# Kernel tuning notes

Hardware: AMD Instinct MI355X
Metric: run time of the kernel (lower is better)

The kernel has to match this reference:

```python
import jax, jax.numpy as jnp
from jax import lax
import numpy as np

N, H, K, B, L = 8192, 256, 100, 32, 128
FS = [1, 2, 3, 4]
W2 = 2 * H + 10  # conv kernel width; padded input width (2H+10) == kernel width -> out width 1


def setup_inputs() -> dict:
    key = jax.random.key(0)
    ks = jax.random.split(key, 16)
    inp = {}
    # scale adj by 1/sqrt(N) so layer1 activations stay O(1) (keeps softmax numerically sane)
    inp["adj"] = jax.random.normal(ks[0], (N, N), jnp.float32) / np.float32(np.sqrt(N))
    # xavier-uniform-scale init for the node embedding parameter
    inp["embedding"] = jax.random.normal(ks[1], (N, H), jnp.float32) * np.float32(np.sqrt(2.0 / (N + H)))
    inp["q_idx"] = jax.random.randint(ks[2], (B, L), 0, N, dtype=jnp.int32)
    inp["a_idx"] = jax.random.randint(ks[3], (B, L), 0, N, dtype=jnp.int32)
    for i, fs in enumerate(FS):
        fan_in = fs * W2
        inp[f"conv_w{i}"] = jax.random.normal(ks[4 + i], (K, 1, fs, W2), jnp.float32) / np.float32(np.sqrt(fan_in))
        inp[f"conv_b{i}"] = jnp.zeros((K,), jnp.float32)
    inp["dense_w"] = jax.random.normal(ks[12], (4 * K * 2, 2), jnp.float32) * np.float32(0.02)
    inp["dense_b"] = jnp.zeros((2,), jnp.float32)
    return inp


def _cnn_branch(t, conv_ws, conv_bs):
    # t: [B, 1, L, 2H]; each conv has padding=5 on both spatial dims,
    # kernel width == 2H+10 so output width == 1; relu then max-pool over full height.
    outs = []
    for w, b in zip(conv_ws, conv_bs):
        y = lax.conv_general_dilated(t, w, (1, 1), [(5, 5), (5, 5)],
                                     dimension_numbers=("NCHW", "OIHW", "NCHW"))
        y = jax.nn.relu(y + b[None, :, None, None])  # [B, K, L+10-fs+1, 1]
        outs.append(jnp.max(y, axis=(2, 3)))  # [B, K]
    return jnp.concatenate(outs, axis=1)  # [B, 4K]


def reference(adj, embedding, q_idx, a_idx,
              conv_w0, conv_b0, conv_w1, conv_b1,
              conv_w2, conv_b2, conv_w3, conv_b3,
              dense_w, dense_b):
    conv_ws = [conv_w0, conv_w1, conv_w2, conv_w3]
    conv_bs = [conv_b0, conv_b1, conv_b2, conv_b3]
    # featureless GCN layer: layer1 = A @ E  -> [N, H]
    layer1 = adj @ embedding
    # per-sample word gathers (ragged in original, fixed length L here)
    Q = layer1[q_idx]  # [B, L, H]
    A = layer1[a_idx]  # [B, L, H]
    # soft alignment: score = Q A^T; wq = softmax rows; wa = softmax(score.T, dim=1) == softmax over axis 1
    score = jnp.einsum("blh,bmh->blm", Q, A)
    wq = jax.nn.softmax(score, axis=2)
    wa = jax.nn.softmax(score, axis=1)
    EQ = jnp.einsum("blm,bmh->blh", wq, A)  # aligned encoding of Q
    EA = jnp.einsum("blm,blh->bmh", wa, Q)  # aligned encoding of A
    # match features: squared diff ++ elementwise product -> [B, 1, L, 2H]
    tq = jnp.concatenate([(Q - EQ) ** 2, Q * EQ], axis=-1)[:, None]
    ta = jnp.concatenate([(A - EA) ** 2, A * EA], axis=-1)[:, None]
    # dropout is identity in eval mode
    q_re = jax.nn.relu(_cnn_branch(tq, conv_ws, conv_bs))  # [B, 4K]
    a_re = jax.nn.relu(_cnn_branch(ta, conv_ws, conv_bs))  # [B, 4K]
    re = jnp.concatenate([q_re, a_re], axis=1)  # [B, 8K]
    logits = re @ dense_w + dense_b  # [B, 2]  (F.relu(score) in original is a discarded no-op)
    return jax.nn.log_softmax(logits, axis=1)
```

## Files before the change

### kernel.cpp

```cpp
#include <hip/hip_runtime.h>
#include <hip/hip_bf16.h>
#include <stdint.h>

typedef unsigned short u16;
typedef __attribute__((ext_vector_type(8))) short bf16x8;
typedef __attribute__((ext_vector_type(4))) float f32x4;

#define NN 8192
#define HH 256
#define KK 100
#define BB 32
#define LL 128
#define SPLITK 8
#define KCH (NN / SPLITK)
#define STEPS1 (KCH / 64)
#define WCATR 1120

__device__ __forceinline__ u16 f2bf_rne(float x) {
  union { __hip_bfloat16 h; u16 u; } v;
  v.h = __float2bfloat16(x);
  return v.u;
}

__device__ __forceinline__ float bf2f(u16 u) {
  union { unsigned int i; float f; } v;
  v.i = ((unsigned int)u) << 16;
  return v.f;
}

__device__ __forceinline__ bf16x8 pack8(f32x4 a, f32x4 b) {
  bf16x8 r;
  r[0] = (short)f2bf_rne(a.x); r[1] = (short)f2bf_rne(a.y);
  r[2] = (short)f2bf_rne(a.z); r[3] = (short)f2bf_rne(a.w);
  r[4] = (short)f2bf_rne(b.x); r[5] = (short)f2bf_rne(b.y);
  r[6] = (short)f2bf_rne(b.z); r[7] = (short)f2bf_rne(b.w);
  return r;
}

__device__ __forceinline__ void gld16(const void* g, void* l) {
  __builtin_amdgcn_global_load_lds(
      (const __attribute__((address_space(1))) unsigned int*)g,
      (__attribute__((address_space(3))) unsigned int*)l, 16, 0, 0);
}

__global__ __launch_bounds__(256) void prep_all(const float* __restrict__ emb,
                                                u16* __restrict__ embT,
                                                const float* __restrict__ w0,
                                                const float* __restrict__ w1,
                                                const float* __restrict__ w2,
                                                const float* __restrict__ w3,
                                                u16* __restrict__ Wcat,
                                                const int* __restrict__ q_idx,
                                                const int* __restrict__ a_idx,
                                                int* __restrict__ rank,
                                                int* __restrict__ rows,
                                                int* __restrict__ muniq) {
  const int bid = blockIdx.x;
  const int tid = threadIdx.x;
  if (bid < 512) {
    __shared__ float t[64][65];
    const int k0 = (bid & 127) * 64, n0 = (bid >> 7) * 64;
#pragma unroll
    for (int i = 0; i < 16; ++i) {
      int idx = i * 256 + tid;
      int r = idx >> 6, c = idx & 63;
      t[r][c] = emb[(size_t)(k0 + r) * HH + n0 + c];
    }
    __syncthreads();
#pragma unroll
    for (int i = 0; i < 16; ++i) {
      int idx = i * 256 + tid;
      int r = idx >> 6, c = idx & 63;
      embT[(size_t)(n0 + r) * NN + k0 + c] = f2bf_rne(t[c][r]);
    }
  } else if (bid < 512 + WCATR) {
    const int kr = bid - 512;
    u16* out = Wcat + (size_t)kr * 512;
    if (kr >= KK * 10) {
      out[tid] = 0;
      out[tid + 256] = 0;
      return;
    }
    const int k = kr / 10, s = kr % 10;
    const float* w;
    int r, fs;
    if (s < 1)      { w = w0; r = s;     fs = 1; }
    else if (s < 3) { w = w1; r = s - 1; fs = 2; }
    else if (s < 6) { w = w2; r = s - 3; fs = 3; }
    else            { w = w3; r = s - 6; fs = 4; }
    const float* src = w + ((size_t)k * fs + r) * 522 + 5;
    out[tid] = f2bf_rne(src[tid]);
    out[tid + 256] = f2bf_rne(src[tid + 256]);
  } else {
    __shared__ unsigned bm[256];
    __shared__ int cnt[256];
    bm[tid] = 0u;
    __syncthreads();
    for (int i = tid; i < BB * LL; i += 256) {
      int q = q_idx[i];
      atomicOr(&bm[q >> 5], 1u << (q & 31));
    }
    for (int i = tid; i < BB * LL; i += 256) {
      int a = a_idx[i];
      atomicOr(&bm[a >> 5], 1u << (a & 31));
    }
    __syncthreads();
    const unsigned w = bm[tid];
    const int myc = __popc(w);
    cnt[tid] = myc;
    __syncthreads();
    for (int off = 1; off < 256; off <<= 1) {
      int v = (tid >= off) ? cnt[tid - off] : 0;
      __syncthreads();
      cnt[tid] += v;
      __syncthreads();
    }
    const int total = cnt[255];
    int base = cnt[tid] - myc;
    for (int j = 0; j < 32; ++j) {
      int n = tid * 32 + j;
      rank[n] = base;
      if ((w >> j) & 1) rows[base++] = n;
    }
    __syncthreads();
    if (tid == 0) *muniq = total;
    if (tid < 128) rows[total + tid] = 0;
  }
}

__global__ __launch_bounds__(512, 6) void gemm_layer1c(const float* __restrict__ adj,
                                                       const u16* __restrict__ embT,
                                                       const int* __restrict__ rows,
                                                       const int* __restrict__ muniq,
                                                       u16* __restrict__ parts) {
  __shared__ __align__(16) float As[64 * 64];
  __shared__ __align__(16) u16 Bs[256 * 64];
  const int tid = threadIdx.x;
  const int lane = tid & 63, wid = tid >> 6;
  const int wm = wid >> 2, wn = wid & 3;
  const int wg = blockIdx.x;
  const int sk = wg & 7;
  const int mt = wg >> 3;
  const int m0 = mt * 64;
  const int M = *muniq;
  if (m0 >= M) return;
  const int kbeg = sk * KCH;

  f32x4 acc[2][4];
  const f32x4 zf = {0.f, 0.f, 0.f, 0.f};
#pragma unroll
  for (int i = 0; i < 2; ++i)
#pragma unroll
    for (int j = 0; j < 4; ++j) acc[i][j] = zf;

  int aRowLoc[2], aGsrc[2];
  const float* aSrc[2];
#pragma unroll
  for (int j = 0; j < 2; ++j) {
    int t = wid * 2 + j;
    aRowLoc[j] = t * 4 + (lane >> 4);
    aGsrc[j] = (lane & 15) ^ (aRowLoc[j] & 15);
    int grow = rows[m0 + aRowLoc[j]];
    aSrc[j] = adj + (size_t)grow * NN + kbeg + aGsrc[j] * 4;
  }
  const u16* bSrc[4];
#pragma unroll
  for (int j = 0; j < 4; ++j) {
    int t = wid * 4 + j;
    int rowB = t * 8 + (lane >> 3);
    int g = (lane & 7) ^ (rowB & 7);
    bSrc[j] = embT + (size_t)rowB * NN + kbeg + g * 8;
  }

  for (int s = 0; s < STEPS1; ++s) {
    const int ks = s * 64;
#pragma unroll
    for (int j = 0; j < 2; ++j)
      gld16(aSrc[j] + ks, (void*)&As[(wid * 2 + j) * 256]);
#pragma unroll
    for (int j = 0; j < 4; ++j)
      gld16(bSrc[j] + ks, (void*)&Bs[(wid * 4 + j) * 512]);
    __syncthreads();
#pragma unroll
    for (int kk = 0; kk < 64; kk += 32) {
      bf16x8 af[2], bfr[4];
      const int g0 = (kk >> 2) + ((lane >> 4) << 1);
#pragma unroll
      for (int mi = 0; mi < 2; ++mi) {
        int row = wm * 32 + mi * 16 + (lane & 15);
        f32x4 p0 = *reinterpret_cast<const f32x4*>(&As[row * 64 + ((g0 ^ (row & 15)) << 2)]);
        f32x4 p1 = *reinterpret_cast<const f32x4*>(&As[row * 64 + (((g0 + 1) ^ (row & 15)) << 2)]);
        af[mi] = pack8(p0, p1);
      }
      const int gb = (kk >> 3) + (lane >> 4);
#pragma unroll
      for (int ni = 0; ni < 4; ++ni) {
        int row = wn * 64 + ni * 16 + (lane & 15);
        bfr[ni] = *reinterpret_cast<const bf16x8*>(&Bs[row * 64 + ((gb ^ (row & 7)) << 3)]);
      }
#pragma unroll
      for (int mi = 0; mi < 2; ++mi)
#pragma unroll
        for (int ni = 0; ni < 4; ++ni)
          acc[mi][ni] = __builtin_amdgcn_mfma_f32_16x16x32_bf16(af[mi], bfr[ni], acc[mi][ni], 0, 0, 0);
    }
    __syncthreads();
  }

  u16* outp = parts + (size_t)sk * ((size_t)NN * HH);
  const int r0 = (lane >> 4) << 2;
  const int coln = wn * 64 + (lane & 15);
#pragma unroll
  for (int mi = 0; mi < 2; ++mi)
#pragma unroll
    for (int ni = 0; ni < 4; ++ni)
#pragma unroll
      for (int r = 0; r < 4; ++r)
        outp[(size_t)(m0 + wm * 32 + mi * 16 + r0 + r) * HH + coln + ni * 16] = f2bf_rne(acc[mi][ni][r]);
}

__global__ __launch_bounds__(256) void gather_qa(const u16* __restrict__ parts,
                                                 const int* __restrict__ q_idx,
                                                 const int* __restrict__ a_idx,
                                                 const int* __restrict__ rank,
                                                 u16* __restrict__ Qbf, u16* __restrict__ Abf) {
  const int rb = blockIdx.x;
  const bool isA = rb >= BB * LL;
  const int r = isA ? rb - BB * LL : rb;
  const int idx = (isA ? a_idx : q_idx)[r];
  const int cidx = rank[idx];
  const int tid = threadIdx.x;
  float s = 0.f;
#pragma unroll
  for (int p = 0; p < SPLITK; ++p)
    s += bf2f(parts[(size_t)p * ((size_t)NN * HH) + (size_t)cidx * HH + tid]);
  (isA ? Abf : Qbf)[(size_t)r * HH + tid] = f2bf_rne(s);
}

__global__ __launch_bounds__(512) void attn_fused(const u16* __restrict__ Qbf,
                                                  const u16* __restrict__ Abf,
                                                  u16* __restrict__ wqbf,
                                                  u16* __restrict__ watbf) {
  __shared__ __align__(16) char lraw[131072];
  u16* Qs = (u16*)lraw;
  u16* As = (u16*)(lraw + 65536);
  float* sc = (float*)lraw;
  const int b = blockIdx.x;
  const int tid = threadIdx.x;
  const int lane = tid & 63, wid = tid >> 6;
  const int wm = wid >> 2, wn = wid & 3;

  const u16* qsrc = Qbf + (size_t)b * (LL * HH);
  const u16* asrc = Abf + (size_t)b * (LL * HH);
#pragma unroll
  for (int i = 0; i < 8; ++i) {
    int gf = i * 512 + tid;
    int l = gf >> 5, g = gf & 31;
    int gp = g ^ (l & 7);
    *reinterpret_cast<bf16x8*>(&Qs[l * 256 + gp * 8]) = *reinterpret_cast<const bf16x8*>(qsrc + l * 256 + g * 8);
    *reinterpret_cast<bf16x8*>(&As[l * 256 + gp * 8]) = *reinterpret_cast<const bf16x8*>(asrc + l * 256 + g * 8);
  }
  __syncthreads();

  f32x4 acc[4][2];
  const f32x4 zf = {0.f, 0.f, 0.f, 0.f};
#pragma unroll
  for (int i = 0; i < 4; ++i)
#pragma unroll
    for (int j = 0; j < 2; ++j) acc[i][j] = zf;

#pragma unroll
  for (int ks = 0; ks < 8; ++ks) {
    bf16x8 af[4], bfr[2];
#pragma unroll
    for (int mi = 0; mi < 4; ++mi) {
      int row = wm * 64 + mi * 16 + (lane & 15);
      int g = ks * 4 + (lane >> 4);
      af[mi] = *reinterpret_cast<const bf16x8*>(&Qs[row * 256 + (g ^ (row & 7)) * 8]);
    }
#pragma unroll
    for (int ni = 0; ni < 2; ++ni) {
      int row = wn * 32 + ni * 16 + (lane & 15);
      int g = ks * 4 + (lane >> 4);
      bfr[ni] = *reinterpret_cast<const bf16x8*>(&As[row * 256 + (g ^ (row & 7)) * 8]);
    }
#pragma unroll
    for (int mi = 0; mi < 4; ++mi)
#pragma unroll
      for (int ni = 0; ni < 2; ++ni)
        acc[mi][ni] = __builtin_amdgcn_mfma_f32_16x16x32_bf16(af[mi], bfr[ni], acc[mi][ni], 0, 0, 0);
  }
  __syncthreads();

  const int r0 = (lane >> 4) << 2;
#pragma unroll
  for (int mi = 0; mi < 4; ++mi)
#pragma unroll
    for (int ni = 0; ni < 2; ++ni) {
      int m = wn * 32 + ni * 16 + (lane & 15);
#pragma unroll
      for (int r = 0; r < 4; ++r) {
        int l = wm * 64 + mi * 16 + r0 + r;
        sc[l * 132 + m] = acc[mi][ni][r];
      }
    }
  __syncthreads();

  {
    const int l = tid >> 2, j = tid & 3;
    const int base = l * 132 + j * 32;
    float mx = -3.4e38f;
#pragma unroll 8
    for (int c = 0; c < 32; ++c) mx = fmaxf(mx, sc[base + c]);
    mx = fmaxf(mx, __shfl_xor(mx, 1));
    mx = fmaxf(mx, __shfl_xor(mx, 2));
    float sum = 0.f;
#pragma unroll 8
    for (int c = 0; c < 32; ++c) sum += expf(sc[base + c] - mx);
    sum += __shfl_xor(sum, 1);
    sum += __shfl_xor(sum, 2);
    float inv = 1.f / sum;
    u16* o = wqbf + (size_t)b * (LL * LL) + l * 128 + j * 32;
#pragma unroll 8
    for (int c = 0; c < 32; ++c) o[c] = f2bf_rne(expf(sc[base + c] - mx) * inv);
  }
  {
    const int m = tid >> 2, j = tid & 3;
    float mx = -3.4e38f;
#pragma unroll 8
    for (int r = 0; r < 32; ++r) mx = fmaxf(mx, sc[(j * 32 + r) * 132 + m]);
    mx = fmaxf(mx, __shfl_xor(mx, 1));
    mx = fmaxf(mx, __shfl_xor(mx, 2));
    float sum = 0.f;
#pragma unroll 8
    for (int r = 0; r < 32; ++r) sum += expf(sc[(j * 32 + r) * 132 + m] - mx);
    sum += __shfl_xor(sum, 1);
    sum += __shfl_xor(sum, 2);
    float inv = 1.f / sum;
    u16* o = watbf + (size_t)b * (LL * LL) + m * 128 + j * 32;
#pragma unroll 8
    for (int r = 0; r < 32; ++r) o[r] = f2bf_rne(expf(sc[(j * 32 + r) * 132 + m] - mx) * inv);
  }
}

__global__ __launch_bounds__(512) void align_mfma(const u16* __restrict__ wqbf,
                                                  const u16* __restrict__ watbf,
                                                  const u16* __restrict__ Qbf,
                                                  const u16* __restrict__ Abf,
                                                  u16* __restrict__ Tbf) {
  __shared__ __align__(16) u16 wsh[128 * 128];
  __shared__ __align__(16) u16 srcT[256 * 140];
  const int bid = blockIdx.x;
  const int side = bid >> 5, b = bid & 31;
  const int tid = threadIdx.x;
  const int lane = tid & 63, wid = tid >> 6;
  const int wm = wid >> 2, wn = wid & 3;

  const u16* wsrc = (side ? watbf : wqbf) + (size_t)b * (LL * LL);
  const u16* ssrc = (side ? Qbf : Abf) + (size_t)b * (LL * HH);
  const u16* msrc = (side ? Abf : Qbf) + (size_t)b * (LL * HH);

#pragma unroll
  for (int i = 0; i < 4; ++i) {
    int gf = i * 512 + tid;
    int row = gf >> 4, g = gf & 15;
    int gp = g ^ (row & 7);
    *reinterpret_cast<bf16x8*>(&wsh[row * 128 + gp * 8]) = *reinterpret_cast<const bf16x8*>(wsrc + row * 128 + g * 8);
  }
#pragma unroll
  for (int i = 0; i < 8; ++i) {
    int gf = i * 512 + tid;
    int j = gf >> 5, g = gf & 31;
    bf16x8 v = *reinterpret_cast<const bf16x8*>(ssrc + j * 256 + g * 8);
#pragma unroll
    for (int e = 0; e < 8; ++e) srcT[(g * 8 + e) * 140 + j] = (u16)v[e];
  }
  __syncthreads();

  f32x4 acc[4][4];
  const f32x4 zf = {0.f, 0.f, 0.f, 0.f};
#pragma unroll
  for (int i = 0; i < 4; ++i)
#pragma unroll
    for (int j = 0; j < 4; ++j) acc[i][j] = zf;

#pragma unroll
  for (int ks = 0; ks < 4; ++ks) {
    bf16x8 af[4], bfr[4];
#pragma unroll
    for (int mi = 0; mi < 4; ++mi) {
      int row = wm * 64 + mi * 16 + (lane & 15);
      int g = ks * 4 + (lane >> 4);
      af[mi] = *reinterpret_cast<const bf16x8*>(&wsh[row * 128 + (g ^ (row & 7)) * 8]);
    }
#pragma unroll
    for (int ni = 0; ni < 4; ++ni) {
      int h = wn * 64 + ni * 16 + (lane & 15);
      int k = ks * 32 + ((lane >> 4) << 3);
      bfr[ni] = *reinterpret_cast<const bf16x8*>(&srcT[h * 140 + k]);
    }
#pragma unroll
    for (int mi = 0; mi < 4; ++mi)
#pragma unroll
      for (int ni = 0; ni < 4; ++ni)
        acc[mi][ni] = __builtin_amdgcn_mfma_f32_16x16x32_bf16(af[mi], bfr[ni], acc[mi][ni], 0, 0, 0);
  }

  u16* outp = Tbf + (size_t)(side * 4096 + b * 128) * 512;
  const int r0 = (lane >> 4) << 2;
#pragma unroll
  for (int mi = 0; mi < 4; ++mi)
#pragma unroll
    for (int ni = 0; ni < 4; ++ni) {
      int h = wn * 64 + ni * 16 + (lane & 15);
#pragma unroll
      for (int r = 0; r < 4; ++r) {
        int i2 = wm * 64 + mi * 16 + r0 + r;
        float mv = bf2f(msrc[(size_t)i2 * HH + h]);
        float e = acc[mi][ni][r];
        float d = mv - e;
        outp[(size_t)i2 * 512 + h] = f2bf_rne(d * d);
        outp[(size_t)i2 * 512 + 256 + h] = f2bf_rne(mv * e);
      }
    }
}

__global__ __launch_bounds__(512, 4) void gemm_conv_red(const u16* __restrict__ Tbf,
                                                        const u16* __restrict__ Wcat,
                                                        const float* __restrict__ b0,
                                                        const float* __restrict__ b1,
                                                        const float* __restrict__ b2,
                                                        const float* __restrict__ b3,
                                                        float* __restrict__ re) {
  __shared__ __align__(16) char smem[41472];
  u16* As = (u16*)smem;
  u16* Bs = (u16*)(smem + 16384);
  u16* Dt = (u16*)smem;
  const int tid = threadIdx.x;
  const int lane = tid & 63, wid = tid >> 6;
  const int wm = wid >> 1, wn = wid & 1;
  const int bx = blockIdx.x;
  const int pair = bx / 7, nt = bx % 7;
  const int sel = pair >> 5, b = pair & 31;
  const int m0 = pair * 128;
  const int n0 = nt * 160;

  f32x4 acc[2][5];
  const f32x4 zf = {0.f, 0.f, 0.f, 0.f};
#pragma unroll
  for (int i = 0; i < 2; ++i)
#pragma unroll
    for (int j = 0; j < 5; ++j) acc[i][j] = zf;

  for (int s = 0; s < 8; ++s) {
    const int ks = s * 64;
#pragma unroll
    for (int j = 0; j < 2; ++j) {
      int t = wid * 2 + j;
      int rowA = t * 8 + (lane >> 3);
      int kA = ((lane & 7) ^ (rowA & 7)) << 3;
      gld16(Tbf + (size_t)(m0 + rowA) * 512 + ks + kA, (void*)&As[t * 512]);
    }
    for (int t = wid; t < 20; t += 8) {
      int rowB = t * 8 + (lane >> 3);
      int kB = ((lane & 7) ^ (rowB & 7)) << 3;
      gld16(Wcat + (size_t)(n0 + rowB) * 512 + ks + kB, (void*)&Bs[t * 512]);
    }
    __syncthreads();
#pragma unroll
    for (int kk = 0; kk < 64; kk += 32) {
      const int k8 = (kk >> 3) + (lane >> 4);
      bf16x8 af[2], bfr[5];
#pragma unroll
      for (int mi = 0; mi < 2; ++mi) {
        int row = wm * 32 + mi * 16 + (lane & 15);
        af[mi] = *reinterpret_cast<const bf16x8*>(&As[row * 64 + ((k8 ^ (row & 7)) << 3)]);
      }
#pragma unroll
      for (int ni = 0; ni < 5; ++ni) {
        int row = wn * 80 + ni * 16 + (lane & 15);
        bfr[ni] = *reinterpret_cast<const bf16x8*>(&Bs[row * 64 + ((k8 ^ (row & 7)) << 3)]);
      }
#pragma unroll
      for (int mi = 0; mi < 2; ++mi)
#pragma unroll
        for (int ni = 0; ni < 5; ++ni)
          acc[mi][ni] = __builtin_amdgcn_mfma_f32_16x16x32_bf16(af[mi], bfr[ni], acc[mi][ni], 0, 0, 0);
    }
    __syncthreads();
  }

  const int r0 = (lane >> 4) << 2;
#pragma unroll
  for (int mi = 0; mi < 2; ++mi)
#pragma unroll
    for (int ni = 0; ni < 5; ++ni) {
      int col = wn * 80 + ni * 16 + (lane & 15);
#pragma unroll
      for (int r = 0; r < 4; ++r)
        Dt[(wm * 32 + mi * 16 + r0 + r) * 162 + col] = f2bf_rne(acc[mi][ni][r]);
    }
  __syncthreads();

  const int offt[4] = {0, 1, 3, 6};
  const int fst[4] = {1, 2, 3, 4};
#pragma unroll
  for (int oi = 0; oi < 8; ++oi) {
    const int o = wid * 8 + oi;
    const int kl = o >> 2, f = o & 3;
    const int kglob = nt * 16 + kl;
    if (kglob >= KK) continue;
    const int fs = fst[f], off = offt[f];
    const float bias = (f == 0 ? b0 : f == 1 ? b1 : f == 2 ? b2 : b3)[kglob];
    const int col = kl * 10 + off;
    const int outh = 139 - fs;
    float best = 0.f;
    for (int i = lane; i < outh; i += 64) {
      float s = bias;
#pragma unroll 4
      for (int r = 0; r < 4; ++r) {
        if (r < fs) {
          int j = i + r - 5;
          if (j >= 0 && j < LL) s += bf2f(Dt[j * 162 + col + r]);
        }
      }
      best = fmaxf(best, s);
    }
    best = fmaxf(best, 0.f);
#pragma unroll
    for (int d = 32; d; d >>= 1) best = fmaxf(best, __shfl_xor(best, d));
    if (lane == 0) re[(size_t)b * 800 + sel * 400 + f * 100 + kglob] = best;
  }
}

__global__ __launch_bounds__(64) void dense_logsm(const float* __restrict__ re,
                                                  const float* __restrict__ dw,
                                                  const float* __restrict__ db,
                                                  float* __restrict__ out) {
  const int b = blockIdx.x;
  const int lane = threadIdx.x;
  const float* r = re + (size_t)b * 800;
  float a0 = 0.f, a1 = 0.f;
  for (int j = lane; j < 800; j += 64) {
    float rv = r[j];
    a0 += rv * dw[j * 2];
    a1 += rv * dw[j * 2 + 1];
  }
#pragma unroll
  for (int d = 32; d; d >>= 1) {
    a0 += __shfl_xor(a0, d);
    a1 += __shfl_xor(a1, d);
  }
  if (lane == 0) {
    a0 += db[0];
    a1 += db[1];
    float mx = fmaxf(a0, a1);
    float lse = mx + logf(expf(a0 - mx) + expf(a1 - mx));
    out[b * 2] = a0 - lse;
    out[b * 2 + 1] = a1 - lse;
  }
}

static const size_t OFF_PARTS = 0;
static const size_t OFF_QBF   = 67108864;
static const size_t OFF_ABF   = OFF_QBF + 2097152;
static const size_t OFF_WQB   = OFF_ABF + 2097152;
static const size_t OFF_WAB   = OFF_WQB + 1048576;
static const size_t OFF_RE    = OFF_WAB + 1048576;
static const size_t OFF_TBF   = OFF_RE + 102400;
static const size_t OFF_WCAT  = OFF_TBF + 8388608;
static const size_t OFF_EMBT  = OFF_WCAT + 1146880;
static const size_t OFF_RANK  = OFF_EMBT + 4194304;
static const size_t OFF_ROWS  = OFF_RANK + 32768;
static const size_t OFF_MUNIQ = OFF_ROWS + 33280;

extern "C" void kernel_launch(void* const* d_in, const int* in_sizes, int n_in,
                              void* d_out, int out_size, void* d_ws, size_t ws_size,
                              hipStream_t stream) {
  (void)in_sizes; (void)n_in; (void)out_size; (void)ws_size;
  const float* adj  = (const float*)d_in[0];
  const float* emb  = (const float*)d_in[1];
  const int* q_idx  = (const int*)d_in[2];
  const int* a_idx  = (const int*)d_in[3];
  const float* cw0 = (const float*)d_in[4];
  const float* cb0 = (const float*)d_in[5];
  const float* cw1 = (const float*)d_in[6];
  const float* cb1 = (const float*)d_in[7];
  const float* cw2 = (const float*)d_in[8];
  const float* cb2 = (const float*)d_in[9];
  const float* cw3 = (const float*)d_in[10];
  const float* cb3 = (const float*)d_in[11];
  const float* dw = (const float*)d_in[12];
  const float* db = (const float*)d_in[13];
  float* out = (float*)d_out;

  char* ws = (char*)d_ws;
  u16* parts   = (u16*)(ws + OFF_PARTS);
  u16* Qbf     = (u16*)(ws + OFF_QBF);
  u16* Abf     = (u16*)(ws + OFF_ABF);
  u16* wqbf    = (u16*)(ws + OFF_WQB);
  u16* watbf   = (u16*)(ws + OFF_WAB);
  float* re    = (float*)(ws + OFF_RE);
  u16* Tbf     = (u16*)(ws + OFF_TBF);
  u16* Wcat    = (u16*)(ws + OFF_WCAT);
  u16* embT    = (u16*)(ws + OFF_EMBT);
  int* rank    = (int*)(ws + OFF_RANK);
  int* rows    = (int*)(ws + OFF_ROWS);
  int* muniq   = (int*)(ws + OFF_MUNIQ);

  prep_all<<<512 + WCATR + 1, 256, 0, stream>>>(emb, embT, cw0, cw1, cw2, cw3, Wcat,
                                                q_idx, a_idx, rank, rows, muniq);
  gemm_layer1c<<<128 * SPLITK, 512, 0, stream>>>(adj, embT, rows, muniq, parts);
  gather_qa<<<2 * BB * LL, 256, 0, stream>>>(parts, q_idx, a_idx, rank, Qbf, Abf);
  attn_fused<<<BB, 512, 0, stream>>>(Qbf, Abf, wqbf, watbf);
  align_mfma<<<64, 512, 0, stream>>>(wqbf, watbf, Qbf, Abf, Tbf);
  gemm_conv_red<<<448, 512, 0, stream>>>(Tbf, Wcat, cb0, cb1, cb2, cb3, re);
  dense_logsm<<<BB, 64, 0, stream>>>(re, dw, db, out);
}
```

Baseline: 132.7 us.

## Halve layer1 GEMM row tile and stage A in 256-wide K groups

Shrinks the M tile of the gathered-row layer1 GEMM from 64 to 32 rows and doubles the grid, so each wave now does one 16-row MFMA strip instead of two. The adjacency tile is loaded in 256-column chunks into a larger swizzled LDS buffer, once per four K steps, while the embedding tile is still reloaded every 64-K step. The aim is more parallelism over the roughly 8K unique rows and fewer barriers and loads for A. In exchange, each embedding tile is reused across fewer rows, so B traffic doubles, and launch bounds drop to 4 blocks per SM because LDS use is higher.

```diff
diff --git a/kernel.cpp b/kernel.cpp
--- a/kernel.cpp
+++ b/kernel.cpp
@@ -13,7 +13,6 @@
 #define LL 128
 #define SPLITK 8
 #define KCH (NN / SPLITK)
-#define STEPS1 (KCH / 64)
 #define WCATR 1120
 
 __device__ __forceinline__ u16 f2bf_rne(float x) {
@@ -128,12 +127,12 @@
   }
 }
 
-__global__ __launch_bounds__(512, 6) void gemm_layer1c(const float* __restrict__ adj,
+__global__ __launch_bounds__(512, 4) void gemm_layer1g(const float* __restrict__ adj,
                                                        const u16* __restrict__ embT,
                                                        const int* __restrict__ rows,
                                                        const int* __restrict__ muniq,
                                                        u16* __restrict__ parts) {
-  __shared__ __align__(16) float As[64 * 64];
+  __shared__ __align__(16) float A4[32 * 256];
   __shared__ __align__(16) u16 Bs[256 * 64];
   const int tid = threadIdx.x;
   const int lane = tid & 63, wid = tid >> 6;
@@ -141,27 +140,22 @@
   const int wg = blockIdx.x;
   const int sk = wg & 7;
   const int mt = wg >> 3;
-  const int m0 = mt * 64;
+  const int m0 = mt * 32;
   const int M = *muniq;
   if (m0 >= M) return;
   const int kbeg = sk * KCH;
 
-  f32x4 acc[2][4];
-  const f32x4 zf = {0.f, 0.f, 0.f, 0.f};
-#pragma unroll
-  for (int i = 0; i < 2; ++i)
-#pragma unroll
-    for (int j = 0; j < 4; ++j) acc[i][j] = zf;
-
-  int aRowLoc[2], aGsrc[2];
-  const float* aSrc[2];
-#pragma unroll
-  for (int j = 0; j < 2; ++j) {
-    int t = wid * 2 + j;
-    aRowLoc[j] = t * 4 + (lane >> 4);
-    aGsrc[j] = (lane & 15) ^ (aRowLoc[j] & 15);
-    int grow = rows[m0 + aRowLoc[j]];
-    aSrc[j] = adj + (size_t)grow * NN + kbeg + aGsrc[j] * 4;
+  f32x4 acc[4];
+#pragma unroll
+  for (int i = 0; i < 4; ++i) acc[i] = (f32x4){0.f, 0.f, 0.f, 0.f};
+
+  const float* aSrc[4];
+#pragma unroll
+  for (int j = 0; j < 4; ++j) {
+    int t = wid * 4 + j;
+    int gsrc = (lane & ~7) | ((lane & 7) ^ (t & 7));
+    int grow = rows[m0 + t];
+    aSrc[j] = adj + (size_t)grow * NN + kbeg + gsrc * 4;
   }
   const u16* bSrc[4];
 #pragma unroll
@@ -172,51 +166,46 @@
     bSrc[j] = embT + (size_t)rowB * NN + kbeg + g * 8;
   }
 
-  for (int s = 0; s < STEPS1; ++s) {
-    const int ks = s * 64;
-#pragma unroll
-    for (int j = 0; j < 2; ++j)
-      gld16(aSrc[j] + ks, (void*)&As[(wid * 2 + j) * 256]);
+  const int arow = wm * 16 + (lane & 15);
+  for (int grp = 0; grp < 4; ++grp) {
 #pragma unroll
     for (int j = 0; j < 4; ++j)
-      gld16(bSrc[j] + ks, (void*)&Bs[(wid * 4 + j) * 512]);
-    __syncthreads();
-#pragma unroll
-    for (int kk = 0; kk < 64; kk += 32) {
-      bf16x8 af[2], bfr[4];
-      const int g0 = (kk >> 2) + ((lane >> 4) << 1);
-#pragma unroll
-      for (int mi = 0; mi < 2; ++mi) {
-        int row = wm * 32 + mi * 16 + (lane & 15);
-        f32x4 p0 = *reinterpret_cast<const f32x4*>(&As[row * 64 + ((g0 ^ (row & 15)) << 2)]);
-        f32x4 p1 = *reinterpret_cast<const f32x4*>(&As[row * 64 + (((g0 + 1) ^ (row & 15)) << 2)]);
-        af[mi] = pack8(p0, p1);
+      gld16(aSrc[j] + grp * 256, (void*)&A4[(wid * 4 + j) * 256]);
+#pragma unroll
+    for (int s = 0; s < 4; ++s) {
+      const int ks = (grp * 4 + s) * 64;
+#pragma unroll
+      for (int j = 0; j < 4; ++j)
+        gld16(bSrc[j] + ks, (void*)&Bs[(wid * 4 + j) * 512]);
+      __syncthreads();
+#pragma unroll
+      for (int kk = 0; kk < 64; kk += 32) {
+        int gk = ((s * 64 + kk) >> 2) + ((lane >> 4) << 1);
+        int s0 = (gk & ~7) | ((gk & 7) ^ (arow & 7));
+        int s1 = ((gk + 1) & ~7) | (((gk + 1) & 7) ^ (arow & 7));
+        f32x4 p0 = *reinterpret_cast<const f32x4*>(&A4[arow * 256 + s0 * 4]);
+        f32x4 p1 = *reinterpret_cast<const f32x4*>(&A4[arow * 256 + s1 * 4]);
+        bf16x8 af = pack8(p0, p1);
+        const int gb = (kk >> 3) + (lane >> 4);
+#pragma unroll
+        for (int ni = 0; ni < 4; ++ni) {
+          int row = wn * 64 + ni * 16 + (lane & 15);
+          bf16x8 bfr = *reinterpret_cast<const bf16x8*>(&Bs[row * 64 + ((gb ^ (row & 7)) << 3)]);
+          acc[ni] = __builtin_amdgcn_mfma_f32_16x16x32_bf16(af, bfr, acc[ni], 0, 0, 0);
+        }
       }
-      const int gb = (kk >> 3) + (lane >> 4);
-#pragma unroll
-      for (int ni = 0; ni < 4; ++ni) {
-        int row = wn * 64 + ni * 16 + (lane & 15);
-        bfr[ni] = *reinterpret_cast<const bf16x8*>(&Bs[row * 64 + ((gb ^ (row & 7)) << 3)]);
-      }
-#pragma unroll
-      for (int mi = 0; mi < 2; ++mi)
-#pragma unroll
-        for (int ni = 0; ni < 4; ++ni)
-          acc[mi][ni] = __builtin_amdgcn_mfma_f32_16x16x32_bf16(af[mi], bfr[ni], acc[mi][ni], 0, 0, 0);
-    }
-    __syncthreads();
+      __syncthreads();
+    }
   }
 
   u16* outp = parts + (size_t)sk * ((size_t)NN * HH);
   const int r0 = (lane >> 4) << 2;
   const int coln = wn * 64 + (lane & 15);
 #pragma unroll
-  for (int mi = 0; mi < 2; ++mi)
-#pragma unroll
-    for (int ni = 0; ni < 4; ++ni)
-#pragma unroll
-      for (int r = 0; r < 4; ++r)
-        outp[(size_t)(m0 + wm * 32 + mi * 16 + r0 + r) * HH + coln + ni * 16] = f2bf_rne(acc[mi][ni][r]);
+  for (int ni = 0; ni < 4; ++ni)
+#pragma unroll
+    for (int r = 0; r < 4; ++r)
+      outp[(size_t)(m0 + wm * 16 + r0 + r) * HH + coln + ni * 16] = f2bf_rne(acc[ni][r]);
 }
 
 __global__ __launch_bounds__(256) void gather_qa(const u16* __restrict__ parts,
@@ -610,7 +599,7 @@
 
   prep_all<<<512 + WCATR + 1, 256, 0, stream>>>(emb, embT, cw0, cw1, cw2, cw3, Wcat,
                                                 q_idx, a_idx, rank, rows, muniq);
-  gemm_layer1c<<<128 * SPLITK, 512, 0, stream>>>(adj, embT, rows, muniq, parts);
+  gemm_layer1g<<<256 * SPLITK, 512, 0, stream>>>(adj, embT, rows, muniq, parts);
   gather_qa<<<2 * BB * LL, 256, 0, stream>>>(parts, q_idx, a_idx, rank, Qbf, Abf);
   attn_fused<<<BB, 512, 0, stream>>>(Qbf, Abf, wqbf, watbf);
   align_mfma<<<64, 512, 0, stream>>>(wqbf, watbf, Qbf, Abf, Tbf);
```

New measurement: 150.3 us. +13.3%, slower.
